# Kernel optimization log

Hardware: AMD Instinct MI355X
Metric: run time of the kernel (lower is better)

## Reference

```python
import jax, jax.numpy as jnp
import numpy as np

NUM_BANDS = 31
POOL_SIZES = (4, 8, 16)
GN_GROUPS = 32
GN_EPS = 1e-5


def _interp_matrix(out_size, in_size):
    # PyTorch bilinear, align_corners=False, as a sparse-ish [out, in] matrix
    i = np.arange(out_size)
    src = (i + 0.5) * (in_size / out_size) - 0.5
    src = np.clip(src, 0.0, in_size - 1)
    lo = np.floor(src).astype(np.int64)
    hi = np.minimum(lo + 1, in_size - 1)
    w = src - lo
    M = np.zeros((out_size, in_size), dtype=np.float32)
    np.add.at(M, (i, lo), 1.0 - w)
    np.add.at(M, (i, hi), w)
    return jnp.asarray(M)


def _scale_branch(x, s, conv_w, spectral_w):
    # x: [B, C, H, W]; adaptive avg pool to (s, s) == uniform pooling (H, W % s == 0)
    B, C, H, W = x.shape
    xp = x.reshape(B, C, s, H // s, s, W // s).mean(axis=(3, 5))  # [B, C, s, s]
    qkv = jnp.einsum('bchw,oc->bohw', xp, conv_w)  # 1x1 conv, no bias
    rd = conv_w.shape[0] // 3
    q, k, v = qkv[:, :rd], qkv[:, rd:2 * rd], qkv[:, 2 * rd:]
    g = rd // NUM_BANDS  # bands_per_group
    S = s * s
    q = q.reshape(B, g, NUM_BANDS, S).transpose(0, 3, 1, 2)  # [B, S, g, n]
    k = k.reshape(B, g, NUM_BANDS, S).transpose(0, 3, 2, 1)  # [B, S, n, g]
    v = v.reshape(B, g, NUM_BANDS, S).transpose(0, 3, 1, 2)  # [B, S, g, n]
    scale = g ** (-0.5)
    attn = jnp.einsum('bsgn,nm,bsmh->bsgh', q, spectral_w, k) * scale  # [B, S, g, g]
    attn = jax.nn.softmax(attn, axis=-1)
    out = jnp.einsum('bsgh,bshn->bsgn', attn, v)  # [B, S, g, n]
    out = out.transpose(0, 2, 3, 1).reshape(B, rd, s, s)
    Mh = _interp_matrix(H, s)
    Mw = _interp_matrix(W, s)
    return jnp.einsum('bcij,hi,wj->bchw', out, Mh, Mw)  # bilinear upsample to [B, rd, H, W]


def _group_norm(x, weight, bias):
    B, C, H, W = x.shape
    xg = x.reshape(B, GN_GROUPS, C // GN_GROUPS, H, W)
    mean = xg.mean(axis=(2, 3, 4), keepdims=True)
    var = ((xg - mean) ** 2).mean(axis=(2, 3, 4), keepdims=True)
    xn = ((xg - mean) * jax.lax.rsqrt(var + GN_EPS)).reshape(B, C, H, W)
    return xn * weight[None, :, None, None] + bias[None, :, None, None]


def setup_inputs() -> dict:
    key = jax.random.key(0)
    ks = jax.random.split(key, 12)
    B, C, H, W = 4, 256, 256, 256
    rd = 93  # reduced_dim for dim=256, reduction=4, num_bands=31
    x = jax.random.normal(ks[0], (B, C, H, W), dtype=jnp.float32)
    conv_ws = [jax.random.normal(ks[1 + i], (3 * rd, C), dtype=jnp.float32) * (C ** -0.5) for i in range(3)]
    sws = [jnp.eye(NUM_BANDS, dtype=jnp.float32) * 0.1
           + 0.01 * jax.random.normal(ks[4 + i], (NUM_BANDS, NUM_BANDS), dtype=jnp.float32) for i in range(3)]
    fusion_w = jax.random.normal(ks[7], (C, 3 * rd), dtype=jnp.float32) * ((3 * rd) ** -0.5)
    fusion_b = jax.random.normal(ks[8], (C,), dtype=jnp.float32) * 0.01
    gn_w = jnp.ones((C,), dtype=jnp.float32) + 0.01 * jax.random.normal(ks[9], (C,), dtype=jnp.float32)
    gn_b = 0.01 * jax.random.normal(ks[10], (C,), dtype=jnp.float32)
    return {'x': x, 'conv_w0': conv_ws[0], 'conv_w1': conv_ws[1], 'conv_w2': conv_ws[2],
            'sw0': sws[0], 'sw1': sws[1], 'sw2': sws[2],
            'fusion_w': fusion_w, 'fusion_b': fusion_b, 'gn_w': gn_w, 'gn_b': gn_b}


def reference(x, conv_w0, conv_w1, conv_w2, sw0, sw1, sw2, fusion_w, fusion_b, gn_w, gn_b):
    conv_ws = (conv_w0, conv_w1, conv_w2)
    sws = (sw0, sw1, sw2)
    scale_outputs = [_scale_branch(x, s, cw, sw) for s, cw, sw in zip(POOL_SIZES, conv_ws, sws)]
    fused = jnp.concatenate(scale_outputs, axis=1)  # [B, 3*rd, H, W]
    out = jnp.einsum('bchw,oc->bohw', fused, fusion_w) + fusion_b[None, :, None, None]
    return _group_norm(out + x, gn_w, gn_b)
```

## Files before the change

kernel.cpp:

```cpp
#include <hip/hip_runtime.h>
#include <hip/hip_bf16.h>
#include <math.h>

#define B 4
#define C 256
#define H 256
#define Wd 256

__global__ __launch_bounds__(256) void xreadproj_kernel(
    const float* __restrict__ x,
    float* __restrict__ pool16, float* __restrict__ xp16o,
    float* __restrict__ xp8o, float* __restrict__ xp4o,
    float* __restrict__ sx) {

    __shared__ float P0[16][72];
    __shared__ float SS16[16][68];
    __shared__ float SS8[16][72];
    __shared__ float SS4[16][80];
    __shared__ float Rs[16 * 29];
    __shared__ float rs[4][2];

    int bc = blockIdx.x;
    int t = threadIdx.x;
    int wg = t >> 6, l = t & 63;

    const float4* xp = (const float4*)(x + (size_t)bc * (H * Wd));

    for (int e = t; e < 576; e += 256) {
        int r = e / 36, g = e - r * 36;
        if (g < 8)       P0[r][64 + g] = 0.f;
        else if (g < 10) SS16[r][g - 8] = 0.f;
        else if (g < 12) SS16[r][56 + g] = 0.f;
        else if (g < 16) SS8[r][g - 12] = 0.f;
        else if (g < 20) SS8[r][52 + g] = 0.f;
        else if (g < 28) SS4[r][g - 20] = 0.f;
        else             SS4[r][44 + g] = 0.f;
    }

    float a16, b16, a8, b8, a4, b4;
    {
        float w0 = 4.f * (float)l + 0.5f;
        float s16v = w0 * 0.0625f - 0.5f;
        if (l <= 1 || l >= 62) { a16 = 0.f; b16 = 0.f; }
        else { a16 = s16v - floorf(s16v); b16 = 0.0625f; }
        float s8v = w0 * 0.03125f - 0.5f;
        if (l <= 3 || l >= 60) { a8 = 0.f; b8 = 0.f; }
        else { a8 = s8v - floorf(s8v); b8 = 0.03125f; }
        float s4v = w0 * 0.015625f - 0.5f;
        if (l <= 7 || l >= 56) { a4 = 0.f; b4 = 0.f; }
        else { a4 = s4v - floorf(s4v); b4 = 0.015625f; }
    }

    const int i16 = t >> 4, j16 = t & 15;
    const int i8 = t >> 3, j8 = t & 7;
    const int i4 = (t - 64) >> 2, j4 = (t - 64) & 3;

    float accA = 0.f;
    float accB = 0.f;
    float sx1 = 0.f, sx2 = 0.f;

    float4 v[4], vn[4];
#pragma unroll
    for (int it = 0; it < 4; ++it)
        v[it] = xp[(wg * 4 + it) * 64 + l];

#pragma unroll 1
    for (int k = 0; k < 16; ++k) {
        if (k > 0) {
            int kk = k - 1;
            if (kk >= i16 - 1 && kk <= i16 + 1) {
#pragma unroll
                for (int rl = 0; rl < 16; ++rl) {
                    float src = ((float)(kk * 16 + rl) + 0.5f) * 0.0625f - 0.5f;
                    src = fminf(fmaxf(src, 0.f), 15.f);
                    int lo = (int)src; float fr = src - (float)lo;
                    float w = (i16 == lo) ? (1.f - fr) : ((i16 == lo + 1) ? fr : 0.f);
                    accA += w * Rs[rl * 29 + j16];
                }
            }
            if (t < 64) {
                if (kk >= 2 * i8 - 1 && kk <= 2 * i8 + 2) {
#pragma unroll
                    for (int rl = 0; rl < 16; ++rl) {
                        float src = ((float)(kk * 16 + rl) + 0.5f) * 0.03125f - 0.5f;
                        src = fminf(fmaxf(src, 0.f), 7.f);
                        int lo = (int)src; float fr = src - (float)lo;
                        float w = (i8 == lo) ? (1.f - fr) : ((i8 == lo + 1) ? fr : 0.f);
                        accB += w * Rs[rl * 29 + 16 + j8];
                    }
                }
            } else if (t < 80) {
                if (kk >= 4 * i4 - 2 && kk <= 4 * i4 + 5) {
#pragma unroll
                    for (int rl = 0; rl < 16; ++rl) {
                        float src = ((float)(kk * 16 + rl) + 0.5f) * 0.015625f - 0.5f;
                        src = fminf(fmaxf(src, 0.f), 3.f);
                        int lo = (int)src; float fr = src - (float)lo;
                        float w = (i4 == lo) ? (1.f - fr) : ((i4 == lo + 1) ? fr : 0.f);
                        accB += w * Rs[rl * 29 + 24 + j4];
                    }
                }
            }
        }

#pragma unroll
        for (int it = 0; it < 4; ++it) {
            int r = wg * 4 + it;
            float4 vv = v[it];
            float p0 = (vv.x + vv.y) + (vv.z + vv.w);
            float pw = fmaf(3.f, vv.w, fmaf(2.f, vv.z, vv.y));
            sx1 += p0;
            sx2 += vv.x * vv.x + vv.y * vv.y + vv.z * vv.z + vv.w * vv.w;
            P0[r][l]       = p0;
            SS16[r][2 + l] = fmaf(b16, pw, a16 * p0);
            SS8[r][4 + l]  = fmaf(b8,  pw, a8  * p0);
            SS4[r][8 + l]  = fmaf(b4,  pw, a4  * p0);
        }

        if (k < 15) {
#pragma unroll
            for (int it = 0; it < 4; ++it)
                vn[it] = xp[((k + 1) * 16 + wg * 4 + it) * 64 + l];
        }
        __syncthreads();

        for (int tk = t; tk < 464; tk += 256) {
            if (tk < 256) {
                int r = tk >> 4, j = tk & 15;
                float sum = 0.f;
#pragma unroll
                for (int q = 0; q < 4; ++q)
                    sum += P0[r][4 * j + 2 + q] - SS16[r][4 * j + 4 + q];
#pragma unroll
                for (int q = 0; q < 4; ++q) sum += SS16[r][4 * j + q];
                if (j == 0) sum += (P0[r][0] - SS16[r][2]) + (P0[r][1] - SS16[r][3]);
                Rs[r * 29 + j] = sum;
            } else if (tk < 384) {
                int q2 = tk - 256; int r = q2 >> 3, j = q2 & 7;
                float sum = 0.f;
#pragma unroll
                for (int q = 0; q < 8; ++q)
                    sum += P0[r][8 * j + 4 + q] - SS8[r][8 * j + 8 + q];
#pragma unroll
                for (int q = 0; q < 8; ++q) sum += SS8[r][8 * j + q];
                if (j == 0) {
#pragma unroll
                    for (int q = 0; q < 4; ++q) sum += P0[r][q] - SS8[r][4 + q];
                }
                Rs[r * 29 + 16 + j] = sum;
            } else if (tk < 448) {
                int q2 = tk - 384; int r = q2 >> 2, j = q2 & 3;
                float sum = 0.f;
#pragma unroll
                for (int q = 0; q < 16; ++q)
                    sum += P0[r][16 * j + 8 + q] - SS4[r][16 * j + 16 + q];
#pragma unroll
                for (int q = 0; q < 16; ++q) sum += SS4[r][16 * j + q];
                if (j == 0) {
#pragma unroll
                    for (int q = 0; q < 8; ++q) sum += P0[r][q] - SS4[r][8 + q];
                }
                Rs[r * 29 + 24 + j] = sum;
            } else {
                int j = tk - 448;
                float sum = 0.f;
#pragma unroll
                for (int r2 = 0; r2 < 16; ++r2) {
#pragma unroll
                    for (int q = 0; q < 4; ++q) sum += P0[r2][4 * j + q];
                }
                pool16[(size_t)bc * 256 + k * 16 + j] = sum * (1.f / 256.f);
            }
        }
        __syncthreads();
#pragma unroll
        for (int it = 0; it < 4; ++it) v[it] = vn[it];
    }

    {
        int kk = 15;
        if (kk >= i16 - 1 && kk <= i16 + 1) {
#pragma unroll
            for (int rl = 0; rl < 16; ++rl) {
                float src = ((float)(kk * 16 + rl) + 0.5f) * 0.0625f - 0.5f;
                src = fminf(fmaxf(src, 0.f), 15.f);
                int lo = (int)src; float fr = src - (float)lo;
                float w = (i16 == lo) ? (1.f - fr) : ((i16 == lo + 1) ? fr : 0.f);
                accA += w * Rs[rl * 29 + j16];
            }
        }
        if (t < 64) {
            if (kk >= 2 * i8 - 1 && kk <= 2 * i8 + 2) {
#pragma unroll
                for (int rl = 0; rl < 16; ++rl) {
                    float src = ((float)(kk * 16 + rl) + 0.5f) * 0.03125f - 0.5f;
                    src = fminf(fmaxf(src, 0.f), 7.f);
                    int lo = (int)src; float fr = src - (float)lo;
                    float w = (i8 == lo) ? (1.f - fr) : ((i8 == lo + 1) ? fr : 0.f);
                    accB += w * Rs[rl * 29 + 16 + j8];
                }
            }
        } else if (t < 80) {
            if (kk >= 4 * i4 - 2 && kk <= 4 * i4 + 5) {
#pragma unroll
                for (int rl = 0; rl < 16; ++rl) {
                    float src = ((float)(kk * 16 + rl) + 0.5f) * 0.015625f - 0.5f;
                    src = fminf(fmaxf(src, 0.f), 3.f);
                    int lo = (int)src; float fr = src - (float)lo;
                    float w = (i4 == lo) ? (1.f - fr) : ((i4 == lo + 1) ? fr : 0.f);
                    accB += w * Rs[rl * 29 + 24 + j4];
                }
            }
        }
    }

    xp16o[(size_t)bc * 256 + t] = accA;
    if (t < 64) xp8o[(size_t)bc * 64 + t] = accB;
    else if (t < 80) xp4o[(size_t)bc * 16 + (t - 64)] = accB;

#pragma unroll
    for (int off = 1; off < 64; off <<= 1) {
        sx1 += __shfl_xor(sx1, off);
        sx2 += __shfl_xor(sx2, off);
    }
    if (l == 0) { rs[wg][0] = sx1; rs[wg][1] = sx2; }
    __syncthreads();
    if (t == 0) {
        sx[bc * 2]     = rs[0][0] + rs[1][0] + rs[2][0] + rs[3][0];
        sx[bc * 2 + 1] = rs[0][1] + rs[1][1] + rs[2][1] + rs[3][1];
    }
}

__global__ __launch_bounds__(256) void site_kernel(
    const float* __restrict__ pool16,
    const float* __restrict__ cw0, const float* __restrict__ cw1,
    const float* __restrict__ cw2,
    const float* __restrict__ sw0, const float* __restrict__ sw1,
    const float* __restrict__ sw2,
    const float* __restrict__ fusion_w,
    float* __restrict__ y4, float* __restrict__ y8, float* __restrict__ y16) {

    __shared__ float P[256];
    __shared__ float Wm[961];
    __shared__ float QKV[279];
    __shared__ float QW[93];
    __shared__ float A[9];
    __shared__ float OUTV[93];

    int t = threadIdx.x;
    int blk = blockIdx.x;
    int b = blk / 336;
    int r = blk % 336;

    int s, site, foff;
    const float* cw; const float* sw; float* yout;
    if (r < 256)      { s = 16; site = r;       cw = cw2; sw = sw2; foff = 186; yout = y16; }
    else if (r < 320) { s = 8;  site = r - 256; cw = cw1; sw = sw1; foff = 93;  yout = y8;  }
    else              { s = 4;  site = r - 320; cw = cw0; sw = sw0; foff = 0;   yout = y4;  }
    int i = site / s, j = site % s;

    for (int idx = t; idx < 961; idx += 256) Wm[idx] = sw[idx];

    {
        int f = 16 / s;
        float acc = 0.f;
        int base = (b * 256 + t) * 256;
        for (int ii = 0; ii < f; ++ii)
            for (int jj = 0; jj < f; ++jj)
                acc += pool16[base + (i * f + ii) * 16 + (j * f + jj)];
        P[t] = acc / (float)(f * f);
    }
    __syncthreads();

    for (int o = t; o < 279; o += 256) {
        const float4* wrow = (const float4*)(cw + o * 256);
        float acc = 0.f;
#pragma unroll 8
        for (int c4 = 0; c4 < 64; ++c4) {
            float4 wv = wrow[c4];
            acc += wv.x * P[c4 * 4] + wv.y * P[c4 * 4 + 1] +
                   wv.z * P[c4 * 4 + 2] + wv.w * P[c4 * 4 + 3];
        }
        QKV[o] = acc;
    }
    __syncthreads();

    if (t < 93) {
        int g = t / 31, m = t % 31;
        float acc = 0.f;
        for (int n = 0; n < 31; ++n) acc += QKV[g * 31 + n] * Wm[n * 31 + m];
        QW[t] = acc;
    }
    __syncthreads();
    if (t < 9) {
        int g = t / 3, h = t % 3;
        float acc = 0.f;
        for (int m = 0; m < 31; ++m) acc += QW[g * 31 + m] * QKV[93 + h * 31 + m];
        A[t] = acc * 0.57735026918962576f;
    }
    __syncthreads();
    if (t < 3) {
        float a0 = A[t * 3], a1 = A[t * 3 + 1], a2 = A[t * 3 + 2];
        float mx = fmaxf(a0, fmaxf(a1, a2));
        float e0 = expf(a0 - mx), e1 = expf(a1 - mx), e2 = expf(a2 - mx);
        float inv = 1.0f / (e0 + e1 + e2);
        A[t * 3] = e0 * inv; A[t * 3 + 1] = e1 * inv; A[t * 3 + 2] = e2 * inv;
    }
    __syncthreads();
    if (t < 93) {
        int g = t / 31, n = t % 31;
        OUTV[t] = A[g * 3] * QKV[186 + n] + A[g * 3 + 1] * QKV[186 + 31 + n] +
                  A[g * 3 + 2] * QKV[186 + 62 + n];
    }
    __syncthreads();
    {
        const float* fr = fusion_w + t * 279 + foff;
        float acc = 0.f;
#pragma unroll 31
        for (int c = 0; c < 93; ++c) acc += fr[c] * OUTV[c];
        yout[(size_t)(b * 256 + t) * (s * s) + site] = acc;
    }
}

__global__ __launch_bounds__(256) void groupstats_kernel(
    const float* __restrict__ y4, const float* __restrict__ y8,
    const float* __restrict__ y16,
    const float* __restrict__ xp4, const float* __restrict__ xp8,
    const float* __restrict__ xp16,
    const float* __restrict__ sx, const float* __restrict__ fusion_b,
    float* __restrict__ stats_g) {

    __shared__ float G1616[256], G168[128], G164[64], G88[64], G84[32], G44[16];
    __shared__ float cs[28];
    __shared__ float ybuf[336], xbuf[336];
    __shared__ float Tm[256];
    __shared__ float red[8];

    int t = threadIdx.x;
    int bg = blockIdx.x;
    int b = bg >> 5, g = bg & 31;

    for (int e = t; e < 588; e += 256) {
        if (e >= 560) {
            int q = e - 560; int sC, iC;
            if (q < 16) { sC = 16; iC = q; }
            else if (q < 24) { sC = 8; iC = q - 16; }
            else { sC = 4; iC = q - 24; }
            int R = 256 / sC;
            int lo = max(0, R * iC - R / 2), hi = min(256, R * iC + (3 * R) / 2);
            float Rinv = 1.f / (float)R, smax = (float)(sC - 1);
            float a = 0.f;
            for (int h = lo; h < hi; ++h) {
                float src = fminf(fmaxf(((float)h + 0.5f) * Rinv - 0.5f, 0.f), smax);
                int lq = (int)src; float fr = src - (float)lq;
                a += (iC == lq) ? (1.f - fr) : ((iC == lq + 1) ? fr : 0.f);
            }
            cs[q] = a;
            continue;
        }
        int sA, sB, iA, iB; float* dst; int off;
        if (e < 256)      { sA = 16; sB = 16; iA = e >> 4; iB = e & 15; dst = G1616; off = e; }
        else if (e < 384) { int q = e - 256; sA = 16; sB = 8; iA = q >> 3; iB = q & 7; dst = G168; off = q; }
        else if (e < 448) { int q = e - 384; sA = 16; sB = 4; iA = q >> 2; iB = q & 3; dst = G164; off = q; }
        else if (e < 512) { int q = e - 448; sA = 8;  sB = 8; iA = q >> 3; iB = q & 7; dst = G88;  off = q; }
        else if (e < 544) { int q = e - 512; sA = 8;  sB = 4; iA = q >> 2; iB = q & 3; dst = G84;  off = q; }
        else              { int q = e - 544; sA = 4;  sB = 4; iA = q >> 2; iB = q & 3; dst = G44;  off = q; }
        int RA = 256 / sA, RB = 256 / sB;
        int lo = max(max(0, RA * iA - RA / 2), RB * iB - RB / 2);
        int hi = min(min(256, RA * iA + (3 * RA) / 2), RB * iB + (3 * RB) / 2);
        float RAi = 1.f / (float)RA, RBi = 1.f / (float)RB;
        float smA = (float)(sA - 1), smB = (float)(sB - 1);
        float a = 0.f;
        for (int h = lo; h < hi; ++h) {
            float sa = fminf(fmaxf(((float)h + 0.5f) * RAi - 0.5f, 0.f), smA);
            int la = (int)sa; float fa = sa - (float)la;
            float wa = (iA == la) ? (1.f - fa) : ((iA == la + 1) ? fa : 0.f);
            float sb = fminf(fmaxf(((float)h + 0.5f) * RBi - 0.5f, 0.f), smB);
            int lb = (int)sb; float fb_ = sb - (float)lb;
            float wb = (iB == lb) ? (1.f - fb_) : ((iB == lb + 1) ? fb_ : 0.f);
            a += wa * wb;
        }
        dst[off] = a;
    }
    __syncthreads();

    double gS1 = 0.0, gS2 = 0.0;

    for (int c8 = 0; c8 < 8; ++c8) {
        int c = g * 8 + c8;
        size_t bc = (size_t)(b * 256 + c);
        ybuf[t] = y16[bc * 256 + t];
        xbuf[t] = xp16[bc * 256 + t];
        if (t < 64) { ybuf[256 + t] = y8[bc * 64 + t]; xbuf[256 + t] = xp8[bc * 64 + t]; }
        else if (t < 80) { ybuf[256 + t] = y4[bc * 16 + (t - 64)]; xbuf[256 + t] = xp4[bc * 16 + (t - 64)]; }
        __syncthreads();

        float pu = 0.f, pv = 0.f;
        for (int e = t; e < 336; e += 256) {
            float yv = ybuf[e];
            pv += 2.f * yv * xbuf[e];
            int ci, cj;
            if (e < 256)      { ci = e >> 4;               cj = e & 15; }
            else if (e < 320) { ci = 16 + ((e - 256) >> 3); cj = 16 + ((e - 256) & 7); }
            else              { ci = 24 + ((e - 320) >> 2); cj = 24 + ((e - 320) & 3); }
            pu += yv * cs[ci] * cs[cj];
        }

        for (int p = 0; p < 6; ++p) {
            const float* Gp; int sA, sB, yAoff, yBoff; float factor;
            switch (p) {
                case 0: Gp = G1616; sA = 16; sB = 16; yAoff = 0;   yBoff = 0;   factor = 1.f; break;
                case 1: Gp = G168;  sA = 16; sB = 8;  yAoff = 0;   yBoff = 256; factor = 2.f; break;
                case 2: Gp = G164;  sA = 16; sB = 4;  yAoff = 0;   yBoff = 320; factor = 2.f; break;
                case 3: Gp = G88;   sA = 8;  sB = 8;  yAoff = 256; yBoff = 256; factor = 1.f; break;
                case 4: Gp = G84;   sA = 8;  sB = 4;  yAoff = 256; yBoff = 320; factor = 2.f; break;
                default:Gp = G44;   sA = 4;  sB = 4;  yAoff = 320; yBoff = 320; factor = 1.f; break;
            }
            __syncthreads();
            int nT = sB * sA;
            if (t < nT) {
                int iB = t / sA, jA = t - iB * sA;
                float a = 0.f;
                for (int jB = 0; jB < sB; ++jB)
                    a += Gp[jA * sB + jB] * ybuf[yBoff + iB * sB + jB];
                Tm[t] = a;
            }
            __syncthreads();
            int nB = sA * sA;
            if (t < nB) {
                int iA = t / sA, jA = t - iA * sA;
                float a = 0.f;
                for (int iB = 0; iB < sB; ++iB)
                    a += Gp[iA * sB + iB] * Tm[iB * sA + jA];
                pv += factor * ybuf[yAoff + t] * a;
            }
        }

#pragma unroll
        for (int off = 1; off < 64; off <<= 1) {
            pu += __shfl_xor(pu, off);
            pv += __shfl_xor(pv, off);
        }
        __syncthreads();
        if ((t & 63) == 0) { red[(t >> 6) * 2] = pu; red[(t >> 6) * 2 + 1] = pv; }
        __syncthreads();
        if (t == 0) {
            float puT = red[0] + red[2] + red[4] + red[6];
            float pvT = red[1] + red[3] + red[5] + red[7];
            float fb = fusion_b[c];
            float s1 = sx[(b * 256 + c) * 2], s2 = sx[(b * 256 + c) * 2 + 1];
            double S1 = (double)s1 + 65536.0 * (double)fb + (double)puT;
            double S2 = (double)s2 + 2.0 * (double)fb * (double)s1 +
                        65536.0 * (double)fb * (double)fb +
                        2.0 * (double)fb * (double)puT + (double)pvT;
            gS1 += S1; gS2 += S2;
        }
        __syncthreads();
    }

    if (t == 0) {
        double mean = gS1 / 524288.0;
        double var  = gS2 / 524288.0 - mean * mean;
        stats_g[bg * 2] = (float)mean;
        stats_g[bg * 2 + 1] = (float)(1.0 / sqrt(var + 1e-5));
    }
}

__global__ __launch_bounds__(256) void write_kernel(
    const float* __restrict__ x,
    const float* __restrict__ ws_y4, const float* __restrict__ ws_y8,
    const float* __restrict__ ws_y16,
    const float* __restrict__ fusion_b,
    const float* __restrict__ gn_w, const float* __restrict__ gn_b,
    const float* __restrict__ stats_g,
    float* __restrict__ out) {

    __shared__ float ly16[256], ly8[64], ly4[16];
    __shared__ float2 rbd16[16][16];
    __shared__ float2 rbd8[16][8];
    __shared__ float2 rbd4[16][4];

    int blk = blockIdx.x;
    int hblk = blk & 15;
    int c = (blk >> 4) & 255;
    int b = blk >> 12;
    int t = threadIdx.x;

    ly16[t] = ws_y16[(size_t)(b * 256 + c) * 256 + t];
    if (t < 64) ly8[t] = ws_y8[(size_t)(b * 256 + c) * 64 + t];
    if (t < 16) ly4[t] = ws_y4[(size_t)(b * 256 + c) * 16 + t];
    __syncthreads();

    for (int idx = t; idx < 448; idx += 256) {
        int r = idx / 28;
        int q = idx - r * 28;
        int h = hblk * 16 + r;
        if (q < 16) {
            float src = (h + 0.5f) * 0.0625f - 0.5f;
            src = fminf(fmaxf(src, 0.f), 15.f);
            int lo = (int)src; float wf = src - lo; int hi = min(lo + 1, 15);
            float rb = (1.f - wf) * ly16[lo * 16 + q] + wf * ly16[hi * 16 + q];
            rbd16[r][q].x = rb;
            if (q > 0) rbd16[r][q - 1].y = rb;
            if (q == 15) rbd16[r][15].y = rb;
        } else if (q < 24) {
            int jj = q - 16;
            float src = (h + 0.5f) * 0.03125f - 0.5f;
            src = fminf(fmaxf(src, 0.f), 7.f);
            int lo = (int)src; float wf = src - lo; int hi = min(lo + 1, 7);
            float rb = (1.f - wf) * ly8[lo * 8 + jj] + wf * ly8[hi * 8 + jj];
            rbd8[r][jj].x = rb;
            if (jj > 0) rbd8[r][jj - 1].y = rb;
            if (jj == 7) rbd8[r][7].y = rb;
        } else {
            int jj = q - 24;
            float src = (h + 0.5f) * 0.015625f - 0.5f;
            src = fminf(fmaxf(src, 0.f), 3.f);
            int lo = (int)src; float wf = src - lo; int hi = min(lo + 1, 3);
            float rb = (1.f - wf) * ly4[lo * 4 + jj] + wf * ly4[hi * 4 + jj];
            rbd4[r][jj].x = rb;
            if (jj > 0) rbd4[r][jj - 1].y = rb;
            if (jj == 3) rbd4[r][3].y = rb;
        }
    }
    __syncthreads();

    int w4 = t & 63;
    int wg = t >> 6;
    int w0 = w4 * 4;

    int jlo16[4], jlo8[4], jlo4[4];
    float ww16[4], ww8[4], ww4[4];
#pragma unroll
    for (int p = 0; p < 4; ++p) {
        int w = w0 + p;
        float s16 = fminf(fmaxf((w + 0.5f) * 0.0625f - 0.5f, 0.f), 15.f);
        jlo16[p] = (int)s16; ww16[p] = s16 - jlo16[p];
        float s8 = fminf(fmaxf((w + 0.5f) * 0.03125f - 0.5f, 0.f), 7.f);
        jlo8[p] = (int)s8; ww8[p] = s8 - jlo8[p];
        float s4 = fminf(fmaxf((w + 0.5f) * 0.015625f - 0.5f, 0.f), 3.f);
        jlo4[p] = (int)s4; ww4[p] = s4 - jlo4[p];
    }

    float fb_c = fusion_b[c];
    int gidx = c >> 3;
    float mean = stats_g[(b * 32 + gidx) * 2];
    float rstd = stats_g[(b * 32 + gidx) * 2 + 1];
    float gwc = gn_w[c], gbc = gn_b[c];

    const float4* xp = (const float4*)(x + (size_t)(b * 256 + c) * (H * Wd));
    float4* op = (float4*)(out + (size_t)(b * 256 + c) * (H * Wd));

#pragma unroll
    for (int it = 0; it < 4; ++it) {
        int r = it * 4 + wg;
        int idx4 = (hblk * 16 + r) * 64 + w4;
        float4 xv = xp[idx4];
        float res[4];
        float px[4] = {xv.x, xv.y, xv.z, xv.w};
#pragma unroll
        for (int p = 0; p < 4; ++p) {
            float f = fb_c;
            float2 v16 = rbd16[r][jlo16[p]];
            f += (1.f - ww16[p]) * v16.x + ww16[p] * v16.y;
            float2 v8 = rbd8[r][jlo8[p]];
            f += (1.f - ww8[p]) * v8.x + ww8[p] * v8.y;
            float2 v4 = rbd4[r][jlo4[p]];
            f += (1.f - ww4[p]) * v4.x + ww4[p] * v4.y;
            float tv = px[p] + f;
            res[p] = (tv - mean) * rstd * gwc + gbc;
        }
        op[idx4] = make_float4(res[0], res[1], res[2], res[3]);
    }
}

extern "C" void kernel_launch(void* const* d_in, const int* in_sizes, int n_in,
                              void* d_out, int out_size, void* d_ws, size_t ws_size,
                              hipStream_t stream) {
    const float* x   = (const float*)d_in[0];
    const float* cw0 = (const float*)d_in[1];
    const float* cw1 = (const float*)d_in[2];
    const float* cw2 = (const float*)d_in[3];
    const float* sw0 = (const float*)d_in[4];
    const float* sw1 = (const float*)d_in[5];
    const float* sw2 = (const float*)d_in[6];
    const float* fw  = (const float*)d_in[7];
    const float* fb  = (const float*)d_in[8];
    const float* gw  = (const float*)d_in[9];
    const float* gb  = (const float*)d_in[10];
    float* out = (float*)d_out;

    float* ws     = (float*)d_ws;
    float* pool16 = ws;
    float* y4     = pool16 + 262144;
    float* y8     = y4 + 16384;
    float* y16    = y8 + 65536;
    float* xp16   = y16 + 262144;
    float* xp8    = xp16 + 262144;
    float* xp4    = xp8 + 65536;
    float* sx     = xp4 + 16384;
    float* statsg = sx + 2048;

    xreadproj_kernel<<<B * C, 256, 0, stream>>>(x, pool16, xp16, xp8, xp4, sx);
    site_kernel<<<B * 336, 256, 0, stream>>>(pool16, cw0, cw1, cw2,
                                             sw0, sw1, sw2, fw, y4, y8, y16);
    groupstats_kernel<<<B * 32, 256, 0, stream>>>(y4, y8, y16, xp4, xp8, xp16,
                                                  sx, fb, statsg);
    write_kernel<<<B * C * 16, 256, 0, stream>>>(x, y4, y8, y16, fb, gw, gb,
                                                 statsg, out);
}
```

Measured before the change: 265.6 us.

## Remove per-tile barriers in x read, split group stats per channel, simplify write math

The x-reading kernel now gives each wavefront its own rows for the row-sum and projection work and keeps partial results per wave. This removes both __syncthreads per 16-row tile and the serial interpolation loops, at the cost of one cross-wave reduction at the end. Group statistics now run as one block per channel followed by a tiny fold kernel, instead of 128 blocks each looping over 8 channels. The write kernel folds the bilinear weights into a base value plus a per-pixel step and the normalisation into a single FMA.

```diff
diff --git a/kernel.cpp b/kernel.cpp
--- a/kernel.cpp
+++ b/kernel.cpp
@@ -17,7 +17,8 @@
     __shared__ float SS16[16][68];
     __shared__ float SS8[16][72];
     __shared__ float SS4[16][80];
-    __shared__ float Rs[16 * 29];
+    __shared__ float Rs[16][29];
+    __shared__ float poolP[16][4][16];
     __shared__ float rs[4][2];
 
     int bc = blockIdx.x;
@@ -51,61 +52,33 @@
         else { a4 = s4v - floorf(s4v); b4 = 0.015625f; }
     }
 
-    const int i16 = t >> 4, j16 = t & 15;
-    const int i8 = t >> 3, j8 = t & 7;
-    const int i4 = (t - 64) >> 2, j4 = (t - 64) & 3;
-
-    float accA = 0.f;
-    float accB = 0.f;
+    const int j16 = l & 15;
+    const int qrow = l >> 4;
+    const int i8 = l >> 3, j8 = l & 7;
+    const int i4l = l >> 2, j4 = l & 3;
+
+    float acc16[4] = {0.f, 0.f, 0.f, 0.f};
+    float acc8 = 0.f, acc4 = 0.f;
     float sx1 = 0.f, sx2 = 0.f;
 
+    __syncthreads();
+
     float4 v[4], vn[4];
 #pragma unroll
     for (int it = 0; it < 4; ++it)
-        v[it] = xp[(wg * 4 + it) * 64 + l];
+        v[it] = xp[(4 * wg + it) * 64 + l];
 
 #pragma unroll 1
     for (int k = 0; k < 16; ++k) {
-        if (k > 0) {
-            int kk = k - 1;
-            if (kk >= i16 - 1 && kk <= i16 + 1) {
-#pragma unroll
-                for (int rl = 0; rl < 16; ++rl) {
-                    float src = ((float)(kk * 16 + rl) + 0.5f) * 0.0625f - 0.5f;
-                    src = fminf(fmaxf(src, 0.f), 15.f);
-                    int lo = (int)src; float fr = src - (float)lo;
-                    float w = (i16 == lo) ? (1.f - fr) : ((i16 == lo + 1) ? fr : 0.f);
-                    accA += w * Rs[rl * 29 + j16];
-                }
-            }
-            if (t < 64) {
-                if (kk >= 2 * i8 - 1 && kk <= 2 * i8 + 2) {
-#pragma unroll
-                    for (int rl = 0; rl < 16; ++rl) {
-                        float src = ((float)(kk * 16 + rl) + 0.5f) * 0.03125f - 0.5f;
-                        src = fminf(fmaxf(src, 0.f), 7.f);
-                        int lo = (int)src; float fr = src - (float)lo;
-                        float w = (i8 == lo) ? (1.f - fr) : ((i8 == lo + 1) ? fr : 0.f);
-                        accB += w * Rs[rl * 29 + 16 + j8];
-                    }
-                }
-            } else if (t < 80) {
-                if (kk >= 4 * i4 - 2 && kk <= 4 * i4 + 5) {
-#pragma unroll
-                    for (int rl = 0; rl < 16; ++rl) {
-                        float src = ((float)(kk * 16 + rl) + 0.5f) * 0.015625f - 0.5f;
-                        src = fminf(fmaxf(src, 0.f), 3.f);
-                        int lo = (int)src; float fr = src - (float)lo;
-                        float w = (i4 == lo) ? (1.f - fr) : ((i4 == lo + 1) ? fr : 0.f);
-                        accB += w * Rs[rl * 29 + 24 + j4];
-                    }
-                }
-            }
+        if (k < 15) {
+#pragma unroll
+            for (int it = 0; it < 4; ++it)
+                vn[it] = xp[((k + 1) * 16 + 4 * wg + it) * 64 + l];
         }
 
 #pragma unroll
         for (int it = 0; it < 4; ++it) {
-            int r = wg * 4 + it;
+            int r = 4 * wg + it;
             float4 vv = v[it];
             float p0 = (vv.x + vv.y) + (vv.z + vv.w);
             float pw = fmaf(3.f, vv.w, fmaf(2.f, vv.z, vv.y));
@@ -117,106 +90,92 @@
             SS4[r][8 + l]  = fmaf(b4,  pw, a4  * p0);
         }
 
-        if (k < 15) {
-#pragma unroll
-            for (int it = 0; it < 4; ++it)
-                vn[it] = xp[((k + 1) * 16 + wg * 4 + it) * 64 + l];
-        }
-        __syncthreads();
-
-        for (int tk = t; tk < 464; tk += 256) {
-            if (tk < 256) {
-                int r = tk >> 4, j = tk & 15;
-                float sum = 0.f;
-#pragma unroll
-                for (int q = 0; q < 4; ++q)
-                    sum += P0[r][4 * j + 2 + q] - SS16[r][4 * j + 4 + q];
-#pragma unroll
-                for (int q = 0; q < 4; ++q) sum += SS16[r][4 * j + q];
-                if (j == 0) sum += (P0[r][0] - SS16[r][2]) + (P0[r][1] - SS16[r][3]);
-                Rs[r * 29 + j] = sum;
-            } else if (tk < 384) {
-                int q2 = tk - 256; int r = q2 >> 3, j = q2 & 7;
-                float sum = 0.f;
-#pragma unroll
-                for (int q = 0; q < 8; ++q)
-                    sum += P0[r][8 * j + 4 + q] - SS8[r][8 * j + 8 + q];
-#pragma unroll
-                for (int q = 0; q < 8; ++q) sum += SS8[r][8 * j + q];
-                if (j == 0) {
-#pragma unroll
-                    for (int q = 0; q < 4; ++q) sum += P0[r][q] - SS8[r][4 + q];
-                }
-                Rs[r * 29 + 16 + j] = sum;
-            } else if (tk < 448) {
-                int q2 = tk - 384; int r = q2 >> 2, j = q2 & 3;
-                float sum = 0.f;
-#pragma unroll
-                for (int q = 0; q < 16; ++q)
-                    sum += P0[r][16 * j + 8 + q] - SS4[r][16 * j + 16 + q];
-#pragma unroll
-                for (int q = 0; q < 16; ++q) sum += SS4[r][16 * j + q];
-                if (j == 0) {
-#pragma unroll
-                    for (int q = 0; q < 8; ++q) sum += P0[r][q] - SS4[r][8 + q];
-                }
-                Rs[r * 29 + 24 + j] = sum;
-            } else {
-                int j = tk - 448;
-                float sum = 0.f;
-#pragma unroll
-                for (int r2 = 0; r2 < 16; ++r2) {
-#pragma unroll
-                    for (int q = 0; q < 4; ++q) sum += P0[r2][4 * j + q];
-                }
-                pool16[(size_t)bc * 256 + k * 16 + j] = sum * (1.f / 256.f);
+        {
+            int r = 4 * wg + (l >> 4), j = l & 15;
+            float sum = 0.f;
+#pragma unroll
+            for (int q = 0; q < 4; ++q)
+                sum += P0[r][4 * j + 2 + q] - SS16[r][4 * j + 4 + q];
+#pragma unroll
+            for (int q = 0; q < 4; ++q) sum += SS16[r][4 * j + q];
+            if (j == 0) sum += (P0[r][0] - SS16[r][2]) + (P0[r][1] - SS16[r][3]);
+            Rs[r][j] = sum;
+        }
+        if (l < 32) {
+            int r = 4 * wg + (l >> 3), j = l & 7;
+            float sum = 0.f;
+#pragma unroll
+            for (int q = 0; q < 8; ++q)
+                sum += P0[r][8 * j + 4 + q] - SS8[r][8 * j + 8 + q];
+#pragma unroll
+            for (int q = 0; q < 8; ++q) sum += SS8[r][8 * j + q];
+            if (j == 0) {
+#pragma unroll
+                for (int q = 0; q < 4; ++q) sum += P0[r][q] - SS8[r][4 + q];
             }
-        }
-        __syncthreads();
-#pragma unroll
-        for (int it = 0; it < 4; ++it) v[it] = vn[it];
-    }
-
-    {
-        int kk = 15;
-        if (kk >= i16 - 1 && kk <= i16 + 1) {
-#pragma unroll
-            for (int rl = 0; rl < 16; ++rl) {
-                float src = ((float)(kk * 16 + rl) + 0.5f) * 0.0625f - 0.5f;
+            Rs[r][16 + j] = sum;
+        } else if (l < 48) {
+            int e = l - 32;
+            int r = 4 * wg + (e >> 2), j = e & 3;
+            float sum = 0.f;
+#pragma unroll
+            for (int q = 0; q < 16; ++q)
+                sum += P0[r][16 * j + 8 + q] - SS4[r][16 * j + 16 + q];
+#pragma unroll
+            for (int q = 0; q < 16; ++q) sum += SS4[r][16 * j + q];
+            if (j == 0) {
+#pragma unroll
+                for (int q = 0; q < 8; ++q) sum += P0[r][q] - SS4[r][8 + q];
+            }
+            Rs[r][24 + j] = sum;
+        } else {
+            int j = l - 48;
+            float sum = 0.f;
+#pragma unroll
+            for (int it2 = 0; it2 < 4; ++it2) {
+#pragma unroll
+                for (int q = 0; q < 4; ++q) sum += P0[4 * wg + it2][4 * j + q];
+            }
+            poolP[k][wg][j] = sum;
+        }
+
+#pragma unroll
+        for (int it2 = 0; it2 < 4; ++it2) {
+            int r = 4 * wg + it2;
+            int grow = 16 * k + r;
+            {
+                float src = ((float)grow + 0.5f) * 0.0625f - 0.5f;
                 src = fminf(fmaxf(src, 0.f), 15.f);
                 int lo = (int)src; float fr = src - (float)lo;
-                float w = (i16 == lo) ? (1.f - fr) : ((i16 == lo + 1) ? fr : 0.f);
-                accA += w * Rs[rl * 29 + j16];
-            }
-        }
-        if (t < 64) {
-            if (kk >= 2 * i8 - 1 && kk <= 2 * i8 + 2) {
-#pragma unroll
-                for (int rl = 0; rl < 16; ++rl) {
-                    float src = ((float)(kk * 16 + rl) + 0.5f) * 0.03125f - 0.5f;
-                    src = fminf(fmaxf(src, 0.f), 7.f);
-                    int lo = (int)src; float fr = src - (float)lo;
-                    float w = (i8 == lo) ? (1.f - fr) : ((i8 == lo + 1) ? fr : 0.f);
-                    accB += w * Rs[rl * 29 + 16 + j8];
+                float Rv = Rs[r][j16];
+#pragma unroll
+                for (int q = 0; q < 4; ++q) {
+                    int iq = 4 * q + qrow;
+                    float w = (iq == lo) ? (1.f - fr) : ((iq == lo + 1) ? fr : 0.f);
+                    acc16[q] = fmaf(w, Rv, acc16[q]);
                 }
             }
-        } else if (t < 80) {
-            if (kk >= 4 * i4 - 2 && kk <= 4 * i4 + 5) {
-#pragma unroll
-                for (int rl = 0; rl < 16; ++rl) {
-                    float src = ((float)(kk * 16 + rl) + 0.5f) * 0.015625f - 0.5f;
-                    src = fminf(fmaxf(src, 0.f), 3.f);
-                    int lo = (int)src; float fr = src - (float)lo;
-                    float w = (i4 == lo) ? (1.f - fr) : ((i4 == lo + 1) ? fr : 0.f);
-                    accB += w * Rs[rl * 29 + 24 + j4];
-                }
+            {
+                float src = ((float)grow + 0.5f) * 0.03125f - 0.5f;
+                src = fminf(fmaxf(src, 0.f), 7.f);
+                int lo = (int)src; float fr = src - (float)lo;
+                float w = (i8 == lo) ? (1.f - fr) : ((i8 == lo + 1) ? fr : 0.f);
+                acc8 = fmaf(w, Rs[r][16 + j8], acc8);
             }
-        }
-    }
-
-    xp16o[(size_t)bc * 256 + t] = accA;
-    if (t < 64) xp8o[(size_t)bc * 64 + t] = accB;
-    else if (t < 80) xp4o[(size_t)bc * 16 + (t - 64)] = accB;
+            {
+                float src = ((float)grow + 0.5f) * 0.015625f - 0.5f;
+                src = fminf(fmaxf(src, 0.f), 3.f);
+                int lo = (int)src; float fr = src - (float)lo;
+                float w = (i4l == lo) ? (1.f - fr) : ((i4l == lo + 1) ? fr : 0.f);
+                acc4 = fmaf(w, Rs[r][24 + j4], acc4);
+            }
+        }
+
+        if (k < 15) {
+#pragma unroll
+            for (int it = 0; it < 4; ++it) v[it] = vn[it];
+        }
+    }
 
 #pragma unroll
     for (int off = 1; off < 64; off <<= 1) {
@@ -224,7 +183,33 @@
         sx2 += __shfl_xor(sx2, off);
     }
     if (l == 0) { rs[wg][0] = sx1; rs[wg][1] = sx2; }
-    __syncthreads();
+
+    __syncthreads();
+
+    float* buf16 = &SS4[0][0];
+    float* buf8  = &SS4[0][0] + 1024;
+    float* buf4  = &P0[0][0];
+
+#pragma unroll
+    for (int q = 0; q < 4; ++q)
+        buf16[wg * 256 + (4 * q + qrow) * 16 + j16] = acc16[q];
+    buf8[wg * 64 + l] = acc8;
+    if (l < 16) buf4[wg * 16 + l] = acc4;
+    __syncthreads();
+
+    xp16o[(size_t)bc * 256 + t] =
+        buf16[t] + buf16[256 + t] + buf16[512 + t] + buf16[768 + t];
+    if (t < 64)
+        xp8o[(size_t)bc * 64 + t] = buf8[t] + buf8[64 + t] + buf8[128 + t] + buf8[192 + t];
+    else if (t < 80) {
+        int e = t - 64;
+        xp4o[(size_t)bc * 16 + e] = buf4[e] + buf4[16 + e] + buf4[32 + e] + buf4[48 + e];
+    }
+    {
+        int k = t >> 4, j = t & 15;
+        pool16[(size_t)bc * 256 + t] =
+            (poolP[k][0][j] + poolP[k][1][j] + poolP[k][2][j] + poolP[k][3][j]) * (1.f / 256.f);
+    }
     if (t == 0) {
         sx[bc * 2]     = rs[0][0] + rs[1][0] + rs[2][0] + rs[3][0];
         sx[bc * 2 + 1] = rs[0][1] + rs[1][1] + rs[2][1] + rs[3][1];
@@ -322,13 +307,13 @@
     }
 }
 
-__global__ __launch_bounds__(256) void groupstats_kernel(
+__global__ __launch_bounds__(256) void chanstat_kernel(
     const float* __restrict__ y4, const float* __restrict__ y8,
     const float* __restrict__ y16,
     const float* __restrict__ xp4, const float* __restrict__ xp8,
     const float* __restrict__ xp16,
     const float* __restrict__ sx, const float* __restrict__ fusion_b,
-    float* __restrict__ stats_g) {
+    double* __restrict__ chanS) {
 
     __shared__ float G1616[256], G168[128], G164[64], G88[64], G84[32], G44[16];
     __shared__ float cs[28];
@@ -337,8 +322,7 @@
     __shared__ float red[8];
 
     int t = threadIdx.x;
-    int bg = blockIdx.x;
-    int b = bg >> 5, g = bg & 31;
+    int bc = blockIdx.x;
 
     for (int e = t; e < 588; e += 256) {
         if (e >= 560) {
@@ -382,88 +366,91 @@
         }
         dst[off] = a;
     }
-    __syncthreads();
-
+
+    size_t bcs = (size_t)bc;
+    ybuf[t] = y16[bcs * 256 + t];
+    xbuf[t] = xp16[bcs * 256 + t];
+    if (t < 64) { ybuf[256 + t] = y8[bcs * 64 + t]; xbuf[256 + t] = xp8[bcs * 64 + t]; }
+    else if (t < 80) { ybuf[256 + t] = y4[bcs * 16 + (t - 64)]; xbuf[256 + t] = xp4[bcs * 16 + (t - 64)]; }
+    __syncthreads();
+
+    float pu = 0.f, pv = 0.f;
+    for (int e = t; e < 336; e += 256) {
+        float yv = ybuf[e];
+        pv += 2.f * yv * xbuf[e];
+        int ci, cj;
+        if (e < 256)      { ci = e >> 4;               cj = e & 15; }
+        else if (e < 320) { ci = 16 + ((e - 256) >> 3); cj = 16 + ((e - 256) & 7); }
+        else              { ci = 24 + ((e - 320) >> 2); cj = 24 + ((e - 320) & 3); }
+        pu += yv * cs[ci] * cs[cj];
+    }
+
+    for (int p = 0; p < 6; ++p) {
+        const float* Gp; int sA, sB, yAoff, yBoff; float factor;
+        switch (p) {
+            case 0: Gp = G1616; sA = 16; sB = 16; yAoff = 0;   yBoff = 0;   factor = 1.f; break;
+            case 1: Gp = G168;  sA = 16; sB = 8;  yAoff = 0;   yBoff = 256; factor = 2.f; break;
+            case 2: Gp = G164;  sA = 16; sB = 4;  yAoff = 0;   yBoff = 320; factor = 2.f; break;
+            case 3: Gp = G88;   sA = 8;  sB = 8;  yAoff = 256; yBoff = 256; factor = 1.f; break;
+            case 4: Gp = G84;   sA = 8;  sB = 4;  yAoff = 256; yBoff = 320; factor = 2.f; break;
+            default:Gp = G44;   sA = 4;  sB = 4;  yAoff = 320; yBoff = 320; factor = 1.f; break;
+        }
+        __syncthreads();
+        int nT = sB * sA;
+        if (t < nT) {
+            int iB = t / sA, jA = t - iB * sA;
+            float a = 0.f;
+            for (int jB = 0; jB < sB; ++jB)
+                a += Gp[jA * sB + jB] * ybuf[yBoff + iB * sB + jB];
+            Tm[t] = a;
+        }
+        __syncthreads();
+        int nB = sA * sA;
+        if (t < nB) {
+            int iA = t / sA, jA = t - iA * sA;
+            float a = 0.f;
+            for (int iB = 0; iB < sB; ++iB)
+                a += Gp[iA * sB + iB] * Tm[iB * sA + jA];
+            pv += factor * ybuf[yAoff + t] * a;
+        }
+    }
+
+#pragma unroll
+    for (int off = 1; off < 64; off <<= 1) {
+        pu += __shfl_xor(pu, off);
+        pv += __shfl_xor(pv, off);
+    }
+    __syncthreads();
+    if ((t & 63) == 0) { red[(t >> 6) * 2] = pu; red[(t >> 6) * 2 + 1] = pv; }
+    __syncthreads();
+    if (t == 0) {
+        float puT = red[0] + red[2] + red[4] + red[6];
+        float pvT = red[1] + red[3] + red[5] + red[7];
+        float fb = fusion_b[bc & 255];
+        float s1 = sx[bc * 2], s2 = sx[bc * 2 + 1];
+        double S1 = (double)s1 + 65536.0 * (double)fb + (double)puT;
+        double S2 = (double)s2 + 2.0 * (double)fb * (double)s1 +
+                    65536.0 * (double)fb * (double)fb +
+                    2.0 * (double)fb * (double)puT + (double)pvT;
+        chanS[bc * 2] = S1;
+        chanS[bc * 2 + 1] = S2;
+    }
+}
+
+__global__ __launch_bounds__(128) void gnfold_kernel(
+    const double* __restrict__ chanS, float* __restrict__ stats_g) {
+    int t = threadIdx.x;
+    int b = t >> 5, g = t & 31;
     double gS1 = 0.0, gS2 = 0.0;
-
     for (int c8 = 0; c8 < 8; ++c8) {
         int c = g * 8 + c8;
-        size_t bc = (size_t)(b * 256 + c);
-        ybuf[t] = y16[bc * 256 + t];
-        xbuf[t] = xp16[bc * 256 + t];
-        if (t < 64) { ybuf[256 + t] = y8[bc * 64 + t]; xbuf[256 + t] = xp8[bc * 64 + t]; }
-        else if (t < 80) { ybuf[256 + t] = y4[bc * 16 + (t - 64)]; xbuf[256 + t] = xp4[bc * 16 + (t - 64)]; }
-        __syncthreads();
-
-        float pu = 0.f, pv = 0.f;
-        for (int e = t; e < 336; e += 256) {
-            float yv = ybuf[e];
-            pv += 2.f * yv * xbuf[e];
-            int ci, cj;
-            if (e < 256)      { ci = e >> 4;               cj = e & 15; }
-            else if (e < 320) { ci = 16 + ((e - 256) >> 3); cj = 16 + ((e - 256) & 7); }
-            else              { ci = 24 + ((e - 320) >> 2); cj = 24 + ((e - 320) & 3); }
-            pu += yv * cs[ci] * cs[cj];
-        }
-
-        for (int p = 0; p < 6; ++p) {
-            const float* Gp; int sA, sB, yAoff, yBoff; float factor;
-            switch (p) {
-                case 0: Gp = G1616; sA = 16; sB = 16; yAoff = 0;   yBoff = 0;   factor = 1.f; break;
-                case 1: Gp = G168;  sA = 16; sB = 8;  yAoff = 0;   yBoff = 256; factor = 2.f; break;
-                case 2: Gp = G164;  sA = 16; sB = 4;  yAoff = 0;   yBoff = 320; factor = 2.f; break;
-                case 3: Gp = G88;   sA = 8;  sB = 8;  yAoff = 256; yBoff = 256; factor = 1.f; break;
-                case 4: Gp = G84;   sA = 8;  sB = 4;  yAoff = 256; yBoff = 320; factor = 2.f; break;
-                default:Gp = G44;   sA = 4;  sB = 4;  yAoff = 320; yBoff = 320; factor = 1.f; break;
-            }
-            __syncthreads();
-            int nT = sB * sA;
-            if (t < nT) {
-                int iB = t / sA, jA = t - iB * sA;
-                float a = 0.f;
-                for (int jB = 0; jB < sB; ++jB)
-                    a += Gp[jA * sB + jB] * ybuf[yBoff + iB * sB + jB];
-                Tm[t] = a;
-            }
-            __syncthreads();
-            int nB = sA * sA;
-            if (t < nB) {
-                int iA = t / sA, jA = t - iA * sA;
-                float a = 0.f;
-                for (int iB = 0; iB < sB; ++iB)
-                    a += Gp[iA * sB + iB] * Tm[iB * sA + jA];
-                pv += factor * ybuf[yAoff + t] * a;
-            }
-        }
-
-#pragma unroll
-        for (int off = 1; off < 64; off <<= 1) {
-            pu += __shfl_xor(pu, off);
-            pv += __shfl_xor(pv, off);
-        }
-        __syncthreads();
-        if ((t & 63) == 0) { red[(t >> 6) * 2] = pu; red[(t >> 6) * 2 + 1] = pv; }
-        __syncthreads();
-        if (t == 0) {
-            float puT = red[0] + red[2] + red[4] + red[6];
-            float pvT = red[1] + red[3] + red[5] + red[7];
-            float fb = fusion_b[c];
-            float s1 = sx[(b * 256 + c) * 2], s2 = sx[(b * 256 + c) * 2 + 1];
-            double S1 = (double)s1 + 65536.0 * (double)fb + (double)puT;
-            double S2 = (double)s2 + 2.0 * (double)fb * (double)s1 +
-                        65536.0 * (double)fb * (double)fb +
-                        2.0 * (double)fb * (double)puT + (double)pvT;
-            gS1 += S1; gS2 += S2;
-        }
-        __syncthreads();
-    }
-
-    if (t == 0) {
-        double mean = gS1 / 524288.0;
-        double var  = gS2 / 524288.0 - mean * mean;
-        stats_g[bg * 2] = (float)mean;
-        stats_g[bg * 2 + 1] = (float)(1.0 / sqrt(var + 1e-5));
-    }
+        gS1 += chanS[(b * 256 + c) * 2];
+        gS2 += chanS[(b * 256 + c) * 2 + 1];
+    }
+    double mean = gS1 / 524288.0;
+    double var  = gS2 / 524288.0 - mean * mean;
+    stats_g[t * 2] = (float)mean;
+    stats_g[t * 2 + 1] = (float)(1.0 / sqrt(var + 1e-5));
 }
 
 __global__ __launch_bounds__(256) void write_kernel(
@@ -527,26 +514,24 @@
 
     int w4 = t & 63;
     int wg = t >> 6;
-    int w0 = w4 * 4;
-
-    int jlo16[4], jlo8[4], jlo4[4];
-    float ww16[4], ww8[4], ww4[4];
-#pragma unroll
-    for (int p = 0; p < 4; ++p) {
-        int w = w0 + p;
-        float s16 = fminf(fmaxf((w + 0.5f) * 0.0625f - 0.5f, 0.f), 15.f);
-        jlo16[p] = (int)s16; ww16[p] = s16 - jlo16[p];
-        float s8 = fminf(fmaxf((w + 0.5f) * 0.03125f - 0.5f, 0.f), 7.f);
-        jlo8[p] = (int)s8; ww8[p] = s8 - jlo8[p];
-        float s4 = fminf(fmaxf((w + 0.5f) * 0.015625f - 0.5f, 0.f), 3.f);
-        jlo4[p] = (int)s4; ww4[p] = s4 - jlo4[p];
-    }
+    float w0 = 4.f * (float)w4 + 0.5f;
+
+    float s16 = fminf(fmaxf(w0 * 0.0625f - 0.5f, 0.f), 15.f);
+    int jlo16 = (int)s16; float w016 = s16 - (float)jlo16;
+    float st16 = (w4 <= 1 || w4 >= 62) ? 0.f : 0.0625f;
+    float s8 = fminf(fmaxf(w0 * 0.03125f - 0.5f, 0.f), 7.f);
+    int jlo8 = (int)s8; float w08 = s8 - (float)jlo8;
+    float st8 = (w4 <= 3 || w4 >= 60) ? 0.f : 0.03125f;
+    float s4 = fminf(fmaxf(w0 * 0.015625f - 0.5f, 0.f), 3.f);
+    int jlo4 = (int)s4; float w04 = s4 - (float)jlo4;
+    float st4 = (w4 <= 7 || w4 >= 56) ? 0.f : 0.015625f;
 
     float fb_c = fusion_b[c];
     int gidx = c >> 3;
     float mean = stats_g[(b * 32 + gidx) * 2];
     float rstd = stats_g[(b * 32 + gidx) * 2 + 1];
-    float gwc = gn_w[c], gbc = gn_b[c];
+    float An = rstd * gn_w[c];
+    float Bn = fmaf(-mean, An, gn_b[c]);
 
     const float4* xp = (const float4*)(x + (size_t)(b * 256 + c) * (H * Wd));
     float4* op = (float4*)(out + (size_t)(b * 256 + c) * (H * Wd));
@@ -555,22 +540,25 @@
     for (int it = 0; it < 4; ++it) {
         int r = it * 4 + wg;
         int idx4 = (hblk * 16 + r) * 64 + w4;
+        float2 v16 = rbd16[r][jlo16];
+        float2 v8 = rbd8[r][jlo8];
+        float2 v4 = rbd4[r][jlo4];
+        float d16 = v16.y - v16.x, d8 = v8.y - v8.x, d4 = v4.y - v4.x;
+        float f0 = fb_c + v16.x + v8.x + v4.x;
+        f0 = fmaf(w016, d16, f0);
+        f0 = fmaf(w08, d8, f0);
+        f0 = fmaf(w04, d4, f0);
+        float c1 = st16 * d16;
+        c1 = fmaf(st8, d8, c1);
+        c1 = fmaf(st4, d4, c1);
+
         float4 xv = xp[idx4];
-        float res[4];
-        float px[4] = {xv.x, xv.y, xv.z, xv.w};
-#pragma unroll
-        for (int p = 0; p < 4; ++p) {
-            float f = fb_c;
-            float2 v16 = rbd16[r][jlo16[p]];
-            f += (1.f - ww16[p]) * v16.x + ww16[p] * v16.y;
-            float2 v8 = rbd8[r][jlo8[p]];
-            f += (1.f - ww8[p]) * v8.x + ww8[p] * v8.y;
-            float2 v4 = rbd4[r][jlo4[p]];
-            f += (1.f - ww4[p]) * v4.x + ww4[p] * v4.y;
-            float tv = px[p] + f;
-            res[p] = (tv - mean) * rstd * gwc + gbc;
-        }
-        op[idx4] = make_float4(res[0], res[1], res[2], res[3]);
+        float4 res;
+        res.x = fmaf(xv.x + f0, An, Bn);
+        res.y = fmaf(xv.y + fmaf(1.f, c1, f0), An, Bn);
+        res.z = fmaf(xv.z + fmaf(2.f, c1, f0), An, Bn);
+        res.w = fmaf(xv.w + fmaf(3.f, c1, f0), An, Bn);
+        op[idx4] = res;
     }
 }
 
@@ -600,12 +588,14 @@
     float* xp4    = xp8 + 65536;
     float* sx     = xp4 + 16384;
     float* statsg = sx + 2048;
+    double* chanS = (double*)(statsg + 256);
 
     xreadproj_kernel<<<B * C, 256, 0, stream>>>(x, pool16, xp16, xp8, xp4, sx);
     site_kernel<<<B * 336, 256, 0, stream>>>(pool16, cw0, cw1, cw2,
                                              sw0, sw1, sw2, fw, y4, y8, y16);
-    groupstats_kernel<<<B * 32, 256, 0, stream>>>(y4, y8, y16, xp4, xp8, xp16,
-                                                  sx, fb, statsg);
+    chanstat_kernel<<<B * C, 256, 0, stream>>>(y4, y8, y16, xp4, xp8, xp16,
+                                               sx, fb, chanS);
+    gnfold_kernel<<<1, 128, 0, stream>>>(chanS, statsg);
     write_kernel<<<B * C * 16, 256, 0, stream>>>(x, y4, y8, y16, fb, gw, gb,
                                                  statsg, out);
 }
```

Result: slower. 275.0 us (+3.6%).
